# Performance work log

Measured on AMD Instinct MI355X. Metric: run time of the kernel, lower is better.

Reference implementation:

```python
import jax, jax.numpy as jnp
import numpy as np

N, F, H, C = 50000, 128, 256, 40
E = 800000
L, J = 3, 2
TOT = 7  # sum_{i<L} J**i


def setup_inputs() -> dict:
    key = jax.random.key(0)
    ks = jax.random.split(key, 16)
    def rn(k, shape, scale):
        return jax.random.normal(k, shape, jnp.float32) * scale
    w = lambda k, shape: rn(k, shape, 1.0 / np.sqrt(shape[0]).astype(np.float32))
    return {
        "x": rn(ks[0], (N, F), 1.0),
        "feature": rn(ks[1], (TOT, N, F), 1.0),
        "src": jax.random.randint(ks[2], (E,), 0, N),
        "dst": jax.random.randint(ks[3], (E,), 0, N),
        "conv_W0": w(ks[4], (F, H)),       "conv_b0": jnp.zeros((H,), jnp.float32),
        "conv_W1": w(ks[5], (2 * H, H)),   "conv_b1": jnp.zeros((H,), jnp.float32),
        "conv_W2": w(ks[6], (2 * H, H)),   "conv_b2": jnp.zeros((H,), jnp.float32),
        "lin_W0": w(ks[7], (F, H)),        "lin_b0": jnp.zeros((H,), jnp.float32),
        "lin_W1": w(ks[8], (2 * F, H)),    "lin_b1": jnp.zeros((H,), jnp.float32),
        "lin_W2": w(ks[9], (4 * F, H)),    "lin_b2": jnp.zeros((H,), jnp.float32),
        "order_weights": rn(ks[10], (J,), 1.0 / np.sqrt(J).astype(np.float32)),
        "cls_W": w(ks[11], (2 * H, C)),    "cls_b": jnp.zeros((C,), jnp.float32),
    }


def reference(x, feature, src, dst,
              conv_W0, conv_b0, conv_W1, conv_b1, conv_W2, conv_b2,
              lin_W0, lin_b0, lin_W1, lin_b1, lin_W2, lin_b2,
              order_weights, cls_W, cls_b):
    # GCN normalization with self-loops (A-hat = D^-1/2 (A+I) D^-1/2)
    loop = jnp.arange(N, dtype=src.dtype)
    src_sl = jnp.concatenate([src, loop])   # [E+N]
    dst_sl = jnp.concatenate([dst, loop])
    deg = jax.ops.segment_sum(jnp.ones_like(dst_sl, jnp.float32), dst_sl, num_segments=N)
    dinv = jax.lax.rsqrt(deg)  # deg >= 1 thanks to self loops
    norm = dinv[src_sl] * dinv[dst_sl]      # [E+N]

    def gcn(h, W, b):
        m = h @ W                            # transform first (smaller gather)
        agg = jax.ops.segment_sum(m[src_sl] * norm[:, None], dst_sl, num_segments=N)
        return agg + b

    conv_W = [conv_W0, conv_W1, conv_W2]
    conv_b = [conv_b0, conv_b1, conv_b2]
    lin_W = [lin_W0, lin_W1, lin_W2]
    lin_b = [lin_b0, lin_b1, lin_b2]

    comb = x
    begin = 0
    for i in range(L):
        convx = jax.nn.relu(gcn(comb, conv_W[i], conv_b[i]))  # [N, H]
        count = J ** i
        lf = feature[begin:begin + count]                      # [count, N, F]
        if i > 0:
            ow = jnp.tile(order_weights, J ** (i - 1)).reshape(-1, 1, 1)
            lf = ow * lf
        lf = jnp.moveaxis(lf, 0, 1).reshape(N, count * F)      # [N, count*F]
        lin_sct = jax.nn.relu(lf @ lin_W[i] + lin_b[i])        # [N, H]
        comb = jnp.concatenate([lin_sct, convx], axis=-1)      # [N, 2H]
        begin += count
    logits = gcn(comb, cls_W, cls_b)                           # [N, C]
    return jax.nn.log_softmax(logits, axis=-1), logits
```

## Files before the change

### kernel.cpp

```cpp
#include <hip/hip_runtime.h>

#define DEVI __device__ __forceinline__

namespace {

constexpr int Nn = 50000;
constexpr int Ne = 800000;
constexpr int Fd = 128;
constexpr int Hd = 256;
constexpr int Cd = 40;
constexpr int NB = (Nn + 255) / 256;

typedef __attribute__((ext_vector_type(8))) short s16x8;
typedef __attribute__((ext_vector_type(8))) unsigned short u16x8;
typedef __attribute__((ext_vector_type(4))) float f32x4;

DEVI unsigned short f2bf(float f) {
  unsigned int u = __builtin_bit_cast(unsigned int, f);
  u += 0x7fffu + ((u >> 16) & 1u);
  return (unsigned short)(u >> 16);
}
DEVI float bf2f(unsigned short s) {
  return __builtin_bit_cast(float, ((unsigned int)s) << 16);
}

DEVI void gld_lds16(const void* gptr, void* lds_base) {
  const unsigned m0v =
      (unsigned)__builtin_amdgcn_readfirstlane((unsigned)(uintptr_t)lds_base);
  asm volatile("s_mov_b32 m0, %0\n\t"
               "global_load_lds_dwordx4 %1, off"
               :: "s"(m0v), "v"(gptr) : "memory");
}

DEVI void wt_one(const float* __restrict__ W, unsigned short* __restrict__ Wt,
                 int idx, int K, int H, const float* __restrict__ ow) {
  int c = idx / K, k = idx - c * K;
  float v = (c < H) ? W[(size_t)k * H + c] : 0.0f;
  if (ow) v *= ow[(k >> 7) & 1];
  Wt[idx] = f2bf(v);
}

constexpr int WTO0 = 0;
constexpr int WTO1 = WTO0 + 256 * 128;
constexpr int WTO2 = WTO1 + 256 * 512;
constexpr int WTO3 = WTO2 + 256 * 512;
constexpr int WTO4 = WTO3 + 256 * 128;
constexpr int WTO5 = WTO4 + 256 * 256;
constexpr int WTO6 = WTO5 + 256 * 512;
constexpr int WTO7 = WTO6 + 64 * 512;
constexpr int PREPTOT = WTO7 + Nn;

__global__ __launch_bounds__(256) void k_prep(
    const float* W0, const float* W1, const float* W2, const float* W3,
    const float* W4, const float* W5, const float* W6, const float* ow,
    unsigned short* T0, unsigned short* T1, unsigned short* T2, unsigned short* T3,
    unsigned short* T4, unsigned short* T5, unsigned short* T6, int* cnt) {
  int idx = blockIdx.x * 256 + threadIdx.x;
  if (idx >= PREPTOT) return;
  if (idx < WTO1)      wt_one(W0, T0, idx - WTO0, 128, 256, nullptr);
  else if (idx < WTO2) wt_one(W1, T1, idx - WTO1, 512, 256, nullptr);
  else if (idx < WTO3) wt_one(W2, T2, idx - WTO2, 512, 256, nullptr);
  else if (idx < WTO4) wt_one(W3, T3, idx - WTO3, 128, 256, nullptr);
  else if (idx < WTO5) wt_one(W4, T4, idx - WTO4, 256, 256, ow);
  else if (idx < WTO6) wt_one(W5, T5, idx - WTO5, 512, 256, ow);
  else if (idx < WTO7) wt_one(W6, T6, idx - WTO6, 512, 40, nullptr);
  else cnt[idx - WTO7] = 0;
}

__global__ void k_count(const int* __restrict__ dst, int* __restrict__ cnt) {
  int e = blockIdx.x * 256 + threadIdx.x;
  if (e < Ne) atomicAdd(&cnt[dst[e]], 1);
}

__global__ __launch_bounds__(256) void k_partial(const int* __restrict__ cnt,
                                                 int* __restrict__ partial) {
  __shared__ int red[256];
  const int t = threadIdx.x;
  const int i = blockIdx.x * 256 + t;
  red[t] = (i < Nn) ? cnt[i] + 1 : 0;
  __syncthreads();
#pragma unroll
  for (int off = 128; off; off >>= 1) {
    if (t < off) red[t] += red[t + off];
    __syncthreads();
  }
  if (t == 0) partial[blockIdx.x] = red[0];
}

__global__ __launch_bounds__(256) void k_scan_small(const int* __restrict__ partial,
                                                    int* __restrict__ poffs,
                                                    int* __restrict__ rowptr) {
  __shared__ int s[256];
  const int t = threadIdx.x;
  const int v = (t < NB) ? partial[t] : 0;
  s[t] = v;
  __syncthreads();
#pragma unroll
  for (int off = 1; off < 256; off <<= 1) {
    int add = (t >= off) ? s[t - off] : 0;
    __syncthreads();
    s[t] += add;
    __syncthreads();
  }
  if (t < NB) poffs[t] = s[t] - v;
  if (t == NB - 1) rowptr[Nn] = s[t];
}

__global__ __launch_bounds__(256) void k_rowptr(const int* __restrict__ cnt,
                                                const int* __restrict__ poffs,
                                                int* __restrict__ rowptr,
                                                int* __restrict__ cursor,
                                                float* __restrict__ dinv) {
  __shared__ int s[256];
  const int t = threadIdx.x;
  const int i = blockIdx.x * 256 + t;
  const int c = (i < Nn) ? cnt[i] + 1 : 0;
  s[t] = c;
  __syncthreads();
#pragma unroll
  for (int off = 1; off < 256; off <<= 1) {
    int add = (t >= off) ? s[t - off] : 0;
    __syncthreads();
    s[t] += add;
    __syncthreads();
  }
  if (i < Nn) {
    const int excl = s[t] - c + poffs[blockIdx.x];
    rowptr[i] = excl;
    cursor[i] = excl;
    dinv[i] = rsqrtf((float)c);
  }
}

__global__ void k_fill(const int* __restrict__ src, const int* __restrict__ dst,
                       const float* __restrict__ dinv, int* __restrict__ cursor,
                       int* __restrict__ csrs, float* __restrict__ csrn) {
  int e = blockIdx.x * 256 + threadIdx.x;
  if (e < Ne) {
    int s = src[e], d = dst[e];
    int pos = atomicAdd(&cursor[d], 1);
    csrs[pos] = s;
    csrn[pos] = dinv[s] * dinv[d];
  } else if (e < Ne + Nn) {
    int d = e - Ne;
    int pos = atomicAdd(&cursor[d], 1);
    csrs[pos] = d;
    float v = dinv[d];
    csrn[pos] = v * v;
  }
}

DEVI void loadB_frags(const unsigned short* __restrict__ Wt, int K, int k0,
                      int colbase, int lane, s16x8 (&bv)[2][4]) {
#pragma unroll
  for (int kk = 0; kk < 2; ++kk)
#pragma unroll
    for (int ni = 0; ni < 4; ++ni) {
      const int col = colbase + ni * 16 + (lane & 15);
      bv[kk][ni] = *(const s16x8*)(Wt + (size_t)col * K + k0 + kk * 32 + (lane >> 4) * 8);
    }
}

struct GRole {
  const float* A;
  const unsigned short* Wt;
  const float* bias;
  unsigned short* C;
  int K;
  int ldc;
  int relu;
};

__global__ __launch_bounds__(256) void k_gemm4(GRole R0, GRole R1, GRole R2, GRole R3) {
  const GRole R = (blockIdx.y == 0) ? R0 : (blockIdx.y == 1) ? R1
                  : (blockIdx.y == 2) ? R2 : R3;
  __shared__ short lA[2][64 * 64];
  const int tid = threadIdx.x;
  const int lane = tid & 63;
  const int wid = tid >> 6;
  const int wc = wid;
  const int row0 = blockIdx.x * 64;
  const size_t NnF = (size_t)Nn * Fd;

  f32x4 acc[4][4];
#pragma unroll
  for (int i = 0; i < 4; ++i)
#pragma unroll
    for (int j = 0; j < 4; ++j) acc[i][j] = (f32x4)0.0f;

  auto loadA = [&](int kt, f32x4 (&A4)[2][2]) {
    const int k0 = kt * 64;
    const int c = k0 >> 7;
    const int f0 = k0 & 127;
#pragma unroll
    for (int i = 0; i < 2; ++i) {
      const int v = tid * 2 + i;
      const int row = v >> 3, c16 = v & 7;
      const int grow = row0 + row;
      const bool rv = grow < Nn;
      const float* p = R.A + (size_t)c * NnF + (size_t)grow * Fd + f0 + c16 * 8;
      A4[i][0] = rv ? *(const f32x4*)p : (f32x4)0.0f;
      A4[i][1] = rv ? *(const f32x4*)(p + 4) : (f32x4)0.0f;
    }
  };
  auto writeA = [&](f32x4 (&A4)[2][2], short* lAb) {
#pragma unroll
    for (int i = 0; i < 2; ++i) {
      const int v = tid * 2 + i;
      const int row = v >> 3, c16 = v & 7;
      s16x8 val;
#pragma unroll
      for (int q = 0; q < 4; ++q) val[q] = (short)f2bf(A4[i][0][q]);
#pragma unroll
      for (int q = 0; q < 4; ++q) val[4 + q] = (short)f2bf(A4[i][1][q]);
      int byte = row * 128 + c16 * 16;
      byte ^= (row & 7) << 4;
      *(s16x8*)((char*)lAb + byte) = val;
    }
  };
  auto compute = [&](const short* lAb, int kt) {
    s16x8 bv[2][4];
    loadB_frags(R.Wt, R.K, kt * 64, wc * 64, lane, bv);
#pragma unroll
    for (int kk = 0; kk < 2; ++kk) {
      s16x8 af[4];
#pragma unroll
      for (int mi = 0; mi < 4; ++mi) {
        int r = mi * 16 + (lane & 15);
        int byte = r * 128 + kk * 64 + (lane >> 4) * 16;
        byte ^= (r & 7) << 4;
        af[mi] = *(const s16x8*)((const char*)lAb + byte);
      }
#pragma unroll
      for (int mi = 0; mi < 4; ++mi)
#pragma unroll
        for (int ni = 0; ni < 4; ++ni)
          acc[mi][ni] = __builtin_amdgcn_mfma_f32_16x16x32_bf16(af[mi], bv[kk][ni], acc[mi][ni], 0, 0, 0);
    }
  };

  const int nkt = R.K >> 6;
  f32x4 Areg[2][2];
  loadA(0, Areg);
  for (int kt = 0; kt < nkt; ++kt) {
    writeA(Areg, lA[kt & 1]);
    if (kt + 1 < nkt) loadA(kt + 1, Areg);
    __syncthreads();
    compute(lA[kt & 1], kt);
  }

#pragma unroll
  for (int ni = 0; ni < 4; ++ni) {
    const int col = wc * 64 + ni * 16 + (lane & 15);
    const float bvl = R.bias ? R.bias[col] : 0.0f;
#pragma unroll
    for (int mi = 0; mi < 4; ++mi) {
      const int rb = row0 + mi * 16 + ((lane >> 4) << 2);
#pragma unroll
      for (int q = 0; q < 4; ++q) {
        int r = rb + q;
        if (r < Nn) {
          float vv = acc[mi][ni][q] + bvl;
          if (R.relu) vv = fmaxf(vv, 0.0f);
          R.C[(size_t)r * R.ldc + col] = f2bf(vv);
        }
      }
    }
  }
}

template <int WRN, int NWC>
__global__ __launch_bounds__(256) void k_gemmB(
    const unsigned short* __restrict__ A, int lda, int K,
    const unsigned short* __restrict__ Wt, unsigned short* __restrict__ C,
    int ldc, int ncols) {
  constexpr int BM = WRN * 64;
  constexpr int AISSW = BM / 32;
  __shared__ short lA[2][BM * 64];
  const int tid = threadIdx.x;
  const int lane = tid & 63;
  const int wid = tid >> 6;
  const int wr = wid / NWC;
  const int wc = wid % NWC;
  const int row0 = blockIdx.x * BM;
  const int c16a = (lane & 7) ^ ((lane >> 3) & 7);

  f32x4 acc[4][4];
#pragma unroll
  for (int i = 0; i < 4; ++i)
#pragma unroll
    for (int j = 0; j < 4; ++j) acc[i][j] = (f32x4)0.0f;

  auto stageA = [&](int kt, short* lAb) {
    const int k0 = kt * 64;
#pragma unroll
    for (int i = 0; i < AISSW; ++i) {
      const int iss = wid * AISSW + i;
      const int row = row0 + iss * 8 + (lane >> 3);
      gld_lds16(A + (size_t)row * lda + k0 + c16a * 8, lAb + iss * 512);
    }
  };
  auto compute = [&](const short* lAb, int kt) {
    s16x8 bv[2][4];
    loadB_frags(Wt, K, kt * 64, wc * 64, lane, bv);
#pragma unroll
    for (int kk = 0; kk < 2; ++kk) {
      s16x8 af[4];
#pragma unroll
      for (int mi = 0; mi < 4; ++mi) {
        int r = wr * 64 + mi * 16 + (lane & 15);
        int byte = r * 128 + kk * 64 + (lane >> 4) * 16;
        byte ^= (r & 7) << 4;
        af[mi] = *(const s16x8*)((const char*)lAb + byte);
      }
#pragma unroll
      for (int mi = 0; mi < 4; ++mi)
#pragma unroll
        for (int ni = 0; ni < 4; ++ni)
          acc[mi][ni] = __builtin_amdgcn_mfma_f32_16x16x32_bf16(af[mi], bv[kk][ni], acc[mi][ni], 0, 0, 0);
    }
  };

  const int nkt = K >> 6;
  stageA(0, lA[0]);
  asm volatile("s_waitcnt vmcnt(0)" ::: "memory");
  __syncthreads();
  for (int kt = 0; kt < nkt; ++kt) {
    if (kt + 1 < nkt) stageA(kt + 1, lA[(kt + 1) & 1]);
    compute(lA[kt & 1], kt);
    asm volatile("s_waitcnt vmcnt(0)" ::: "memory");
    __syncthreads();
  }

#pragma unroll
  for (int ni = 0; ni < 4; ++ni) {
    const int col = wc * 64 + ni * 16 + (lane & 15);
    if (col >= ncols) continue;
#pragma unroll
    for (int mi = 0; mi < 4; ++mi) {
      const int rb = row0 + wr * 64 + mi * 16 + ((lane >> 4) << 2);
#pragma unroll
      for (int q = 0; q < 4; ++q) {
        int r = rb + q;
        if (r < Nn) C[(size_t)r * ldc + col] = f2bf(acc[mi][ni][q]);
      }
    }
  }
}

__global__ __launch_bounds__(256) void k_gather(
    const unsigned short* __restrict__ m, const int* __restrict__ rowptr,
    const int* __restrict__ csrs, const float* __restrict__ csrn,
    const float* __restrict__ bias, unsigned short* __restrict__ outp,
    int ldc, int col_off) {
  const int wid = (blockIdx.x * 256 + threadIdx.x) >> 6;
  const int lane = threadIdx.x & 63;
  if (wid >= Nn) return;
  const int half = lane >> 5;
  const int sub = lane & 31;
  const int e0 = rowptr[wid], e1 = rowptr[wid + 1];
  const unsigned short* mcol = m + sub * 8;
  float acc[8];
#pragma unroll
  for (int q = 0; q < 8; ++q) acc[q] = 0.f;

  for (int base = e0; base < e1; base += 64) {
    const int idx = base + lane;
    int s_ = 0;
    float w_ = 0.f;
    if (idx < e1) { s_ = csrs[idx]; w_ = csrn[idx]; }
    const int cn = min(64, e1 - base);
    const int npair = (cn + 1) >> 1;
    float w0, w1, w2, w3;
    u16x8 v0, v1, v2, v3;
    auto pick = [&](int p, float& w, u16x8& v) {
      if (p < npair) {
        const int j = 2 * p + half;
        const int ss = __shfl(s_, j);
        w = __shfl(w_, j);
        v = *(const u16x8*)(mcol + (size_t)ss * Hd);
      } else { w = 0.f; v = (u16x8)0; }
    };
    pick(0, w0, v0); pick(1, w1, v1); pick(2, w2, v2); pick(3, w3, v3);
    for (int p0 = 0; p0 < npair; p0 += 4) {
#pragma unroll
      for (int q = 0; q < 8; ++q) acc[q] += w0 * bf2f(v0[q]);
      pick(p0 + 4, w0, v0);
#pragma unroll
      for (int q = 0; q < 8; ++q) acc[q] += w1 * bf2f(v1[q]);
      pick(p0 + 5, w1, v1);
#pragma unroll
      for (int q = 0; q < 8; ++q) acc[q] += w2 * bf2f(v2[q]);
      pick(p0 + 6, w2, v2);
#pragma unroll
      for (int q = 0; q < 8; ++q) acc[q] += w3 * bf2f(v3[q]);
      pick(p0 + 7, w3, v3);
    }
  }

#pragma unroll
  for (int q = 0; q < 8; ++q) acc[q] += __shfl_xor(acc[q], 32);
  if (half == 0) {
    u16x8 o;
#pragma unroll
    for (int q = 0; q < 8; ++q) {
      float v = fmaxf(acc[q] + bias[sub * 8 + q], 0.f);
      o[q] = f2bf(v);
    }
    *(u16x8*)(outp + (size_t)wid * ldc + col_off + sub * 8) = o;
  }
}

__global__ __launch_bounds__(256) void k_gcls(
    const unsigned short* __restrict__ mc, const int* __restrict__ rowptr,
    const int* __restrict__ csrs, const float* __restrict__ csrn,
    const float* __restrict__ clsb, float* __restrict__ outp) {
  const int wid = (blockIdx.x * 256 + threadIdx.x) >> 6;
  const int lane = threadIdx.x & 63;
  if (wid >= Nn) return;
  const int half = lane >> 5;
  const int sub = lane & 31;
  const bool act = sub < 5;
  const int e0 = rowptr[wid], e1 = rowptr[wid + 1];
  float acc[8];
#pragma unroll
  for (int q = 0; q < 8; ++q) acc[q] = 0.f;

  for (int base = e0; base < e1; base += 64) {
    const int idx = base + lane;
    int s_ = 0;
    float w_ = 0.f;
    if (idx < e1) { s_ = csrs[idx]; w_ = csrn[idx]; }
    const int cn = min(64, e1 - base);
    const int npair = (cn + 1) >> 1;
    int sA = __shfl(s_, half);
    float wA = __shfl(w_, half);
    u16x8 vA = act ? *(const u16x8*)(mc + (size_t)sA * Cd + sub * 8) : (u16x8)0;
    for (int jj = 1; jj < npair; ++jj) {
      const int j = 2 * jj + half;
      const int sB = __shfl(s_, j);
      const float wB = __shfl(w_, j);
      const u16x8 vB = act ? *(const u16x8*)(mc + (size_t)sB * Cd + sub * 8) : (u16x8)0;
#pragma unroll
      for (int q = 0; q < 8; ++q) acc[q] += wA * bf2f(vA[q]);
      wA = wB; vA = vB;
    }
#pragma unroll
    for (int q = 0; q < 8; ++q) acc[q] += wA * bf2f(vA[q]);
  }

#pragma unroll
  for (int q = 0; q < 8; ++q) acc[q] += __shfl_xor(acc[q], 32);

  float l[8];
  float mx = -3.4e38f;
  if (act) {
#pragma unroll
    for (int q = 0; q < 8; ++q) {
      l[q] = acc[q] + clsb[sub * 8 + q];
      mx = fmaxf(mx, l[q]);
    }
  }
#pragma unroll
  for (int off = 1; off < 8; off <<= 1) mx = fmaxf(mx, __shfl_xor(mx, off));
  float se = 0.f;
  if (act) {
#pragma unroll
    for (int q = 0; q < 8; ++q) se += expf(l[q] - mx);
  }
#pragma unroll
  for (int off = 1; off < 8; off <<= 1) se += __shfl_xor(se, off);
  const float lse = mx + logf(se);
  if (half == 0 && act) {
    float* o1 = outp + (size_t)wid * Cd + sub * 8;
    float* o2 = o1 + (size_t)Nn * Cd;
#pragma unroll
    for (int q = 0; q < 8; ++q) {
      o1[q] = l[q] - lse;
      o2[q] = l[q];
    }
  }
}

}

extern "C" void kernel_launch(void* const* d_in, const int* in_sizes, int n_in,
                              void* d_out, int out_size, void* d_ws, size_t ws_size,
                              hipStream_t stream) {
  (void)in_sizes; (void)n_in; (void)out_size; (void)ws_size;
  const float* x       = (const float*)d_in[0];
  const float* feature = (const float*)d_in[1];
  const int* src       = (const int*)d_in[2];
  const int* dst       = (const int*)d_in[3];
  const float* convW[3] = {(const float*)d_in[4], (const float*)d_in[6], (const float*)d_in[8]};
  const float* convB[3] = {(const float*)d_in[5], (const float*)d_in[7], (const float*)d_in[9]};
  const float* linW[3]  = {(const float*)d_in[10], (const float*)d_in[12], (const float*)d_in[14]};
  const float* linB[3]  = {(const float*)d_in[11], (const float*)d_in[13], (const float*)d_in[15]};
  const float* oweights = (const float*)d_in[16];
  const float* clsW     = (const float*)d_in[17];
  const float* clsB     = (const float*)d_in[18];
  float* out = (float*)d_out;

  char* wsp = (char*)d_ws;
  auto alloc = [&](size_t bytes) -> void* {
    void* p = wsp;
    wsp += (bytes + 255) & ~(size_t)255;
    return p;
  };
  int* cnt      = (int*)alloc((size_t)Nn * 4);
  int* cursor   = (int*)alloc((size_t)Nn * 4);
  int* rowptr   = (int*)alloc((size_t)(Nn + 1) * 4);
  float* dinv   = (float*)alloc((size_t)Nn * 4);
  int* partial  = (int*)alloc((size_t)NB * 4);
  int* poffs    = (int*)alloc((size_t)NB * 4);
  int* csrs     = (int*)alloc((size_t)(Ne + Nn) * 4);
  float* csrn   = (float*)alloc((size_t)(Ne + Nn) * 4);
  unsigned short* WtC0 = (unsigned short*)alloc((size_t)256 * 128 * 2);
  unsigned short* WtC1 = (unsigned short*)alloc((size_t)256 * 512 * 2);
  unsigned short* WtC2 = (unsigned short*)alloc((size_t)256 * 512 * 2);
  unsigned short* WtL0 = (unsigned short*)alloc((size_t)256 * 128 * 2);
  unsigned short* WtL1 = (unsigned short*)alloc((size_t)256 * 256 * 2);
  unsigned short* WtL2 = (unsigned short*)alloc((size_t)256 * 512 * 2);
  unsigned short* WtCl = (unsigned short*)alloc((size_t)64 * 512 * 2);
  unsigned short* mbuf = (unsigned short*)alloc((size_t)Nn * Hd * 2);
  unsigned short* mcls = (unsigned short*)alloc((size_t)Nn * Cd * 2);
  unsigned short* comb0 = (unsigned short*)alloc((size_t)(Nn + 256) * 512 * 2);
  unsigned short* comb1 = (unsigned short*)alloc((size_t)(Nn + 256) * 512 * 2);
  unsigned short* comb2 = (unsigned short*)alloc((size_t)(Nn + 256) * 512 * 2);

  k_prep<<<(PREPTOT + 255) / 256, 256, 0, stream>>>(
      convW[0], convW[1], convW[2], linW[0], linW[1], linW[2], clsW, oweights,
      WtC0, WtC1, WtC2, WtL0, WtL1, WtL2, WtCl, cnt);
  k_count<<<(Ne + 255) / 256, 256, 0, stream>>>(dst, cnt);
  k_partial<<<NB, 256, 0, stream>>>(cnt, partial);
  k_scan_small<<<1, 256, 0, stream>>>(partial, poffs, rowptr);
  k_rowptr<<<NB, 256, 0, stream>>>(cnt, poffs, rowptr, cursor, dinv);
  k_fill<<<(Ne + Nn + 255) / 256, 256, 0, stream>>>(src, dst, dinv, cursor, csrs, csrn);

  const int GM = (Nn + 63) / 64;
  const int GC = (Nn + 255) / 256;
  const int GB = (Nn * 64) / 256;

  GRole rConv0{x,                              WtC0, nullptr, mbuf,  128, Hd,  0};
  GRole rLin0 {feature,                        WtL0, linB[0], comb0, 128, 512, 1};
  GRole rLin1 {feature + (size_t)1 * Nn * Fd,  WtL1, linB[1], comb1, 256, 512, 1};
  GRole rLin2 {feature + (size_t)3 * Nn * Fd,  WtL2, linB[2], comb2, 512, 512, 1};
  k_gemm4<<<dim3(GM, 4), 256, 0, stream>>>(rConv0, rLin0, rLin1, rLin2);

  k_gather<<<GB, 256, 0, stream>>>(mbuf, rowptr, csrs, csrn, convB[0], comb0, 512, 256);
  k_gemmB<1, 4><<<GM, 256, 0, stream>>>(comb0, 512, 512, WtC1, mbuf, Hd, 256);
  k_gather<<<GB, 256, 0, stream>>>(mbuf, rowptr, csrs, csrn, convB[1], comb1, 512, 256);
  k_gemmB<1, 4><<<GM, 256, 0, stream>>>(comb1, 512, 512, WtC2, mbuf, Hd, 256);
  k_gather<<<GB, 256, 0, stream>>>(mbuf, rowptr, csrs, csrn, convB[2], comb2, 512, 256);
  k_gemmB<4, 1><<<GC, 256, 0, stream>>>(comb2, 512, 512, WtCl, mcls, Cd, 40);
  k_gcls<<<GB, 256, 0, stream>>>(mcls, rowptr, csrs, csrn, clsB, out);
}
```

Baseline: 585.1 us.

## Stage weight tiles in LDS with pre-swizzled layout instead of per-wave global loads

Both GEMM kernels now load the weight (B) tile into shared memory with direct global-to-LDS loads, then read MFMA fragments from LDS. Previously each wave read its B fragments straight from global memory. The weight-transpose prep kernel pre-applies the XOR swizzle so the LDS reads avoid bank conflicts. In exchange, A double-buffering is removed and two barriers per k-step are added, which serialises load and compute and may expose more memory latency.

```diff
diff --git a/kernel.cpp b/kernel.cpp
--- a/kernel.cpp
+++ b/kernel.cpp
@@ -35,8 +35,10 @@
 DEVI void wt_one(const float* __restrict__ W, unsigned short* __restrict__ Wt,
                  int idx, int K, int H, const float* __restrict__ ow) {
   int c = idx / K, k = idx - c * K;
-  float v = (c < H) ? W[(size_t)k * H + c] : 0.0f;
-  if (ow) v *= ow[(k >> 7) & 1];
+  int kt = k >> 6, c16 = (k >> 3) & 7, j = k & 7;
+  int ksrc = (kt << 6) | ((c16 ^ (c & 7)) << 3) | j;
+  float v = (c < H) ? W[(size_t)ksrc * H + c] : 0.0f;
+  if (ow) v *= ow[(ksrc >> 7) & 1];
   Wt[idx] = f2bf(v);
 }
 
@@ -150,17 +152,6 @@
   }
 }
 
-DEVI void loadB_frags(const unsigned short* __restrict__ Wt, int K, int k0,
-                      int colbase, int lane, s16x8 (&bv)[2][4]) {
-#pragma unroll
-  for (int kk = 0; kk < 2; ++kk)
-#pragma unroll
-    for (int ni = 0; ni < 4; ++ni) {
-      const int col = colbase + ni * 16 + (lane & 15);
-      bv[kk][ni] = *(const s16x8*)(Wt + (size_t)col * K + k0 + kk * 32 + (lane >> 4) * 8);
-    }
-}
-
 struct GRole {
   const float* A;
   const unsigned short* Wt;
@@ -174,7 +165,8 @@
 __global__ __launch_bounds__(256) void k_gemm4(GRole R0, GRole R1, GRole R2, GRole R3) {
   const GRole R = (blockIdx.y == 0) ? R0 : (blockIdx.y == 1) ? R1
                   : (blockIdx.y == 2) ? R2 : R3;
-  __shared__ short lA[2][64 * 64];
+  __shared__ short lA[64 * 64];
+  __shared__ short lB[256 * 64];
   const int tid = threadIdx.x;
   const int lane = tid & 63;
   const int wid = tid >> 6;
@@ -203,7 +195,7 @@
       A4[i][1] = rv ? *(const f32x4*)(p + 4) : (f32x4)0.0f;
     }
   };
-  auto writeA = [&](f32x4 (&A4)[2][2], short* lAb) {
+  auto writeA = [&](f32x4 (&A4)[2][2]) {
 #pragma unroll
     for (int i = 0; i < 2; ++i) {
       const int v = tid * 2 + i;
@@ -215,27 +207,41 @@
       for (int q = 0; q < 4; ++q) val[4 + q] = (short)f2bf(A4[i][1][q]);
       int byte = row * 128 + c16 * 16;
       byte ^= (row & 7) << 4;
-      *(s16x8*)((char*)lAb + byte) = val;
-    }
-  };
-  auto compute = [&](const short* lAb, int kt) {
-    s16x8 bv[2][4];
-    loadB_frags(R.Wt, R.K, kt * 64, wc * 64, lane, bv);
+      *(s16x8*)((char*)lA + byte) = val;
+    }
+  };
+  auto stageB = [&](int kt) {
+    const int k0 = kt * 64;
+#pragma unroll
+    for (int i = 0; i < 8; ++i) {
+      const int iss = wid * 8 + i;
+      const int col = iss * 8 + (lane >> 3);
+      gld_lds16(R.Wt + (size_t)col * R.K + k0 + (lane & 7) * 8, lB + iss * 512);
+    }
+  };
+  auto compute = [&]() {
 #pragma unroll
     for (int kk = 0; kk < 2; ++kk) {
-      s16x8 af[4];
+      s16x8 af[4], bv[4];
 #pragma unroll
       for (int mi = 0; mi < 4; ++mi) {
         int r = mi * 16 + (lane & 15);
         int byte = r * 128 + kk * 64 + (lane >> 4) * 16;
         byte ^= (r & 7) << 4;
-        af[mi] = *(const s16x8*)((const char*)lAb + byte);
+        af[mi] = *(const s16x8*)((const char*)lA + byte);
       }
 #pragma unroll
+      for (int ni = 0; ni < 4; ++ni) {
+        int c = wc * 64 + ni * 16 + (lane & 15);
+        int byte = c * 128 + kk * 64 + (lane >> 4) * 16;
+        byte ^= (c & 7) << 4;
+        bv[ni] = *(const s16x8*)((const char*)lB + byte);
+      }
+#pragma unroll
       for (int mi = 0; mi < 4; ++mi)
 #pragma unroll
         for (int ni = 0; ni < 4; ++ni)
-          acc[mi][ni] = __builtin_amdgcn_mfma_f32_16x16x32_bf16(af[mi], bv[kk][ni], acc[mi][ni], 0, 0, 0);
+          acc[mi][ni] = __builtin_amdgcn_mfma_f32_16x16x32_bf16(af[mi], bv[ni], acc[mi][ni], 0, 0, 0);
     }
   };
 
@@ -243,10 +249,17 @@
   f32x4 Areg[2][2];
   loadA(0, Areg);
   for (int kt = 0; kt < nkt; ++kt) {
-    writeA(Areg, lA[kt & 1]);
-    if (kt + 1 < nkt) loadA(kt + 1, Areg);
-    __syncthreads();
-    compute(lA[kt & 1], kt);
+    writeA(Areg);
+    stageB(kt);
+    if (kt + 1 < nkt) {
+      loadA(kt + 1, Areg);
+      asm volatile("s_waitcnt vmcnt(4)" ::: "memory");
+    } else {
+      asm volatile("s_waitcnt vmcnt(0)" ::: "memory");
+    }
+    __syncthreads();
+    compute();
+    __syncthreads();
   }
 
 #pragma unroll
@@ -275,8 +288,11 @@
     const unsigned short* __restrict__ Wt, unsigned short* __restrict__ C,
     int ldc, int ncols) {
   constexpr int BM = WRN * 64;
+  constexpr int BN = NWC * 64;
   constexpr int AISSW = BM / 32;
-  __shared__ short lA[2][BM * 64];
+  constexpr int BISSW = BN / 32;
+  __shared__ short lA[BM * 64];
+  __shared__ short lB[BN * 64];
   const int tid = threadIdx.x;
   const int lane = tid & 63;
   const int wid = tid >> 6;
@@ -291,44 +307,53 @@
 #pragma unroll
     for (int j = 0; j < 4; ++j) acc[i][j] = (f32x4)0.0f;
 
-  auto stageA = [&](int kt, short* lAb) {
+  auto stage = [&](int kt) {
     const int k0 = kt * 64;
 #pragma unroll
     for (int i = 0; i < AISSW; ++i) {
       const int iss = wid * AISSW + i;
       const int row = row0 + iss * 8 + (lane >> 3);
-      gld_lds16(A + (size_t)row * lda + k0 + c16a * 8, lAb + iss * 512);
-    }
-  };
-  auto compute = [&](const short* lAb, int kt) {
-    s16x8 bv[2][4];
-    loadB_frags(Wt, K, kt * 64, wc * 64, lane, bv);
+      gld_lds16(A + (size_t)row * lda + k0 + c16a * 8, lA + iss * 512);
+    }
+#pragma unroll
+    for (int i = 0; i < BISSW; ++i) {
+      const int iss = wid * BISSW + i;
+      const int col = iss * 8 + (lane >> 3);
+      gld_lds16(Wt + (size_t)col * K + k0 + (lane & 7) * 8, lB + iss * 512);
+    }
+  };
+  auto compute = [&]() {
 #pragma unroll
     for (int kk = 0; kk < 2; ++kk) {
-      s16x8 af[4];
+      s16x8 af[4], bv[4];
 #pragma unroll
       for (int mi = 0; mi < 4; ++mi) {
         int r = wr * 64 + mi * 16 + (lane & 15);
         int byte = r * 128 + kk * 64 + (lane >> 4) * 16;
         byte ^= (r & 7) << 4;
-        af[mi] = *(const s16x8*)((const char*)lAb + byte);
+        af[mi] = *(const s16x8*)((const char*)lA + byte);
       }
 #pragma unroll
+      for (int ni = 0; ni < 4; ++ni) {
+        int c = wc * 64 + ni * 16 + (lane & 15);
+        int byte = c * 128 + kk * 64 + (lane >> 4) * 16;
+        byte ^= (c & 7) << 4;
+        bv[ni] = *(const s16x8*)((const char*)lB + byte);
+      }
+#pragma unroll
       for (int mi = 0; mi < 4; ++mi)
 #pragma unroll
         for (int ni = 0; ni < 4; ++ni)
-          acc[mi][ni] = __builtin_amdgcn_mfma_f32_16x16x32_bf16(af[mi], bv[kk][ni], acc[mi][ni], 0, 0, 0);
+          acc[mi][ni] = __builtin_amdgcn_mfma_f32_16x16x32_bf16(af[mi], bv[ni], acc[mi][ni], 0, 0, 0);
     }
   };
 
   const int nkt = K >> 6;
-  stageA(0, lA[0]);
-  asm volatile("s_waitcnt vmcnt(0)" ::: "memory");
-  __syncthreads();
   for (int kt = 0; kt < nkt; ++kt) {
-    if (kt + 1 < nkt) stageA(kt + 1, lA[(kt + 1) & 1]);
-    compute(lA[kt & 1], kt);
+    stage(kt);
     asm volatile("s_waitcnt vmcnt(0)" ::: "memory");
+    __syncthreads();
+    compute();
     __syncthreads();
   }
 
```

New measurement: 534.8 us. 8.6% less time.
